# Kernel optimization log

Hardware: AMD Instinct MI355X
Metric: run time of the kernel (lower is better)

Reference implementation:

```python
import jax, jax.numpy as jnp
import numpy as np

# Dims (match init_kwargs)
B, N, D_MODEL = 64, 64, 512
D_STATE = 512
D_ATT = D_MODEL
H, W, C, K = 128, 128, 16, 5
T = 32  # num_steps
HALF = K // 2


def _lin(key, out_d, in_d):
    kw, kb = jax.random.split(key)
    w = jax.random.normal(kw, (out_d, in_d), jnp.float32) * 0.02
    b = jax.random.normal(kb, (out_d,), jnp.float32) * 0.02
    return w, b


def setup_inputs() -> dict:
    key = jax.random.key(0)
    ks = jax.random.split(key, 12)
    token_reps = jax.random.normal(ks[0], (B, N, D_MODEL), jnp.float32)
    global_rep = jax.random.normal(ks[1], (B, D_MODEL), jnp.float32)
    attention_mask = jnp.ones((B, N), jnp.int32)
    w_init, b_init = _lin(ks[2], D_STATE, D_MODEL)
    wq, bq = _lin(ks[3], D_ATT, D_STATE)
    wk, bk = _lin(ks[4], D_ATT, D_MODEL)
    wv, bv = _lin(ks[5], D_ATT, D_MODEL)
    gru_in = D_ATT + D_MODEL
    w_ih, b_ih = _lin(ks[6], 3 * D_STATE, gru_in)
    w_hh, b_hh = _lin(ks[7], 3 * D_STATE, D_STATE)
    w_write, b_write = _lin(ks[8], C * K * K, D_STATE + D_ATT)
    w_loc, b_loc = _lin(ks[9], 3, D_STATE + D_ATT + D_MODEL)
    return dict(token_reps=token_reps, global_rep=global_rep, attention_mask=attention_mask,
                w_init=w_init, b_init=b_init, wq=wq, bq=bq, wk=wk, bk=bk, wv=wv, bv=bv,
                w_ih=w_ih, b_ih=b_ih, w_hh=w_hh, b_hh=b_hh,
                w_write=w_write, b_write=b_write, w_loc=w_loc, b_loc=b_loc)


def _forward(token_reps, global_rep, attention_mask,
             w_init, b_init, wq, bq, wk, bk, wv, bv,
             w_ih, b_ih, w_hh, b_hh, w_write, b_write, w_loc, b_loc):
    Bv = token_reps.shape[0]
    # Precompute keys/values (constant over steps)
    k_tok = token_reps @ wk.T + bk  # [B,N,d_att]
    v_tok = token_reps @ wv.T + bv  # [B,N,d_att]
    invalid = attention_mask == 0

    s0 = jnp.tanh(global_rep @ w_init.T + b_init)  # [B,d_state]
    # Padded canvas (NHWC): full KxK patches always fit; crop at the end
    # reproduces the torch clipped-window write exactly.
    canvas0 = jnp.zeros((Bv, H + 2 * HALF, W + 2 * HALF, C), jnp.float32)
    b_idx = jnp.arange(Bv)
    koff = jnp.arange(K)

    def step(carry, _):
        s, canvas_p = carry
        q = s @ wq.T + bq  # [B,d_att]
        scores = jnp.einsum('bd,bnd->bn', q, k_tok)
        scores = jnp.where(invalid, -1e9, scores)
        alpha = jax.nn.softmax(scores, axis=-1)
        r = jnp.einsum('bn,bnd->bd', alpha, v_tok)  # [B,d_att]
        # GRUCell (torch gate order r,z,n)
        x = jnp.concatenate([r, global_rep], axis=-1)
        gi = x @ w_ih.T + b_ih
        gh = s @ w_hh.T + b_hh
        ir, iz, inn = jnp.split(gi, 3, axis=-1)
        hr, hz, hn = jnp.split(gh, 3, axis=-1)
        rg = jax.nn.sigmoid(ir + hr)
        zg = jax.nn.sigmoid(iz + hz)
        ng = jnp.tanh(inn + rg * hn)
        s_new = (1.0 - zg) * ng + zg * s
        # Write patch
        patch = (jnp.concatenate([s_new, r], axis=-1) @ w_write.T + b_write)
        patch = patch.reshape(Bv, C, K, K).transpose(0, 2, 3, 1)  # [B,K,K,C]
        loc = jnp.concatenate([s_new, r, global_rep], axis=-1) @ w_loc.T + b_loc
        cx = jnp.tanh(loc[:, 0])
        cy = jnp.tanh(loc[:, 1])
        j = jnp.clip(jnp.round(0.5 * (cx + 1.0) * (W - 1)), 0, W - 1).astype(jnp.int32)
        i = jnp.clip(jnp.round(0.5 * (cy + 1.0) * (H - 1)), 0, H - 1).astype(jnp.int32)
        # padded coords: top-left of window in padded canvas is (i, j)
        rows = i[:, None] + koff  # [B,K]
        cols = j[:, None] + koff  # [B,K]
        canvas_p = canvas_p.at[b_idx[:, None, None], rows[:, :, None], cols[:, None, :]].add(patch)
        return (s_new, canvas_p), None

    (_, canvas_p), _ = jax.lax.scan(step, (s0, canvas0), None, length=T)
    canvas = canvas_p[:, HALF:HALF + H, HALF:HALF + W, :].transpose(0, 3, 1, 2)  # [B,C,H,W]
    return canvas


def reference(token_reps, global_rep, attention_mask,
              w_init, b_init, wq, bq, wk, bk, wv, bv,
              w_ih, b_ih, w_hh, b_hh, w_write, b_write, w_loc, b_loc):
    return _forward(token_reps, global_rep, attention_mask,
                    w_init, b_init, wq, bq, wk, bk, wv, bv,
                    w_ih, b_ih, w_hh, b_hh, w_write, b_write, w_loc, b_loc)
```

## Files before the change

kernel.cpp:

```cpp
#include <hip/hip_runtime.h>

#define BB 64
#define DD 512
#define TT 32

__device__ __forceinline__ float dot4(const float4 a, const float4 b) {
  return a.x * b.x + a.y * b.y + a.z * b.z + a.w * b.w;
}

__device__ __forceinline__ void cst(float* p, float v) {
  __hip_atomic_store(p, v, __ATOMIC_RELAXED, __HIP_MEMORY_SCOPE_AGENT);
}

__global__ void vecs_k(const float* __restrict__ wq, const float* __restrict__ bk,
                       const float* __restrict__ wk, const float* __restrict__ bq,
                       float* __restrict__ kqb, float* __restrict__ wkbq,
                       float* __restrict__ bqbk, unsigned* __restrict__ bar) {
  const int tid = threadIdx.x, bz = blockIdx.x;
  if (bz < 2) {
    const int d = bz * 256 + tid;
    float s = 0.f;
    for (int e = 0; e < DD; ++e) s += wq[e * DD + d] * bk[e];
    kqb[d] = s;
  } else {
    const int k = (bz - 2) * 256 + tid;
    float s = 0.f;
    for (int e = 0; e < DD; ++e) s += bq[e] * wk[e * DD + k];
    wkbq[k] = s;
    if (bz == 2 && tid == 0) {
      float t2 = 0.f;
      for (int e = 0; e < DD; ++e) t2 += bq[e] * bk[e];
      *bqbk = t2;
    }
    if (bz == 3) {
      if (tid < 16)
        __hip_atomic_store(bar + tid * 64, 0u, __ATOMIC_RELAXED, __HIP_MEMORY_SCOPE_AGENT);
      __hip_atomic_store(bar + 1024 + tid * 32, 0u, __ATOMIC_RELAXED, __HIP_MEMORY_SCOPE_AGENT);
    }
  }
}

__global__ __launch_bounds__(256) void gemm128_k(
    const float* __restrict__ A, int lda, int a_trans,
    const float* __restrict__ B, int ldb, int boff, int b_trans,
    const float* __restrict__ bias, float* __restrict__ C, long c_stride_z, int ldc,
    int kfrom, int klen, int act) {
  __shared__ __align__(16) float As[16][132];
  __shared__ __align__(16) float Bs[16][68];
  const int tid = threadIdx.x;
  const int tx = tid & 15, ty = tid >> 4;
  const int m0 = blockIdx.x * 128, n0 = blockIdx.y * 64;
  const int kbase = kfrom + blockIdx.z * klen;
  float* Ce = C + (long)blockIdx.z * c_stride_z;
  float acc[8][4];
#pragma unroll
  for (int i = 0; i < 8; ++i)
#pragma unroll
    for (int j = 0; j < 4; ++j) acc[i][j] = 0.f;

  for (int k0 = kbase; k0 < kbase + klen; k0 += 16) {
    if (!a_trans) {
      const int row = tid >> 1, half = tid & 1;
      const float* ap = A + (long)(m0 + row) * lda + k0 + half * 8;
      const float4 a0 = *(const float4*)ap;
      const float4 a1 = *(const float4*)(ap + 4);
      const int kb = half * 8;
      As[kb + 0][row] = a0.x; As[kb + 1][row] = a0.y; As[kb + 2][row] = a0.z; As[kb + 3][row] = a0.w;
      As[kb + 4][row] = a1.x; As[kb + 5][row] = a1.y; As[kb + 6][row] = a1.z; As[kb + 7][row] = a1.w;
    } else {
      const int kk = tid >> 4, mseg = tid & 15;
      const float* ap = A + (long)(k0 + kk) * lda + m0 + mseg * 8;
      *(float4*)&As[kk][mseg * 8] = *(const float4*)ap;
      *(float4*)&As[kk][mseg * 8 + 4] = *(const float4*)(ap + 4);
    }
    if (!b_trans) {
      const int n = tid >> 2, q = tid & 3;
      const float4 b0 = *(const float4*)(B + (long)(n0 + n) * ldb + boff + k0 + q * 4);
      Bs[q * 4 + 0][n] = b0.x; Bs[q * 4 + 1][n] = b0.y; Bs[q * 4 + 2][n] = b0.z; Bs[q * 4 + 3][n] = b0.w;
    } else {
      const int kk = tid >> 4, nq = tid & 15;
      *(float4*)&Bs[kk][nq * 4] = *(const float4*)(B + (long)(k0 + kk) * ldb + boff + n0 + nq * 4);
    }
    __syncthreads();
#pragma unroll
    for (int kk = 0; kk < 16; ++kk) {
      const float4 a0 = *(const float4*)&As[kk][ty * 8];
      const float4 a1 = *(const float4*)&As[kk][ty * 8 + 4];
      const float4 b0 = *(const float4*)&Bs[kk][tx * 4];
      const float am[8] = {a0.x, a0.y, a0.z, a0.w, a1.x, a1.y, a1.z, a1.w};
#pragma unroll
      for (int i = 0; i < 8; ++i) {
        acc[i][0] += am[i] * b0.x; acc[i][1] += am[i] * b0.y;
        acc[i][2] += am[i] * b0.z; acc[i][3] += am[i] * b0.w;
      }
    }
    __syncthreads();
  }
  float4 bv = make_float4(0.f, 0.f, 0.f, 0.f);
  if (bias) bv = *(const float4*)(bias + n0 + tx * 4);
#pragma unroll
  for (int i = 0; i < 8; ++i) {
    const int m = m0 + ty * 8 + i;
    float4 v = make_float4(acc[i][0] + bv.x, acc[i][1] + bv.y, acc[i][2] + bv.z, acc[i][3] + bv.w);
    if (act == 1) { v.x = tanhf(v.x); v.y = tanhf(v.y); v.z = tanhf(v.z); v.w = tanhf(v.w); }
    *(float4*)&Ce[(long)m * ldc + n0 + tx * 4] = v;
  }
}

__global__ __launch_bounds__(256) void gemm128_dual_k(
    const float* __restrict__ A,
    const float* __restrict__ B0, const float* __restrict__ bias0, float* __restrict__ C0,
    const float* __restrict__ B1, const float* __restrict__ bias1, float* __restrict__ C1) {
  __shared__ __align__(16) float As[16][132];
  __shared__ __align__(16) float Bs[16][68];
  const int tid = threadIdx.x;
  const int tx = tid & 15, ty = tid >> 4;
  const int m0 = blockIdx.x * 128, n0 = blockIdx.y * 64;
  const float* B = blockIdx.z ? B1 : B0;
  const float* bias = blockIdx.z ? bias1 : bias0;
  float* C = blockIdx.z ? C1 : C0;
  float acc[8][4];
#pragma unroll
  for (int i = 0; i < 8; ++i)
#pragma unroll
    for (int j = 0; j < 4; ++j) acc[i][j] = 0.f;

  for (int k0 = 0; k0 < 512; k0 += 16) {
    {
      const int row = tid >> 1, half = tid & 1;
      const float* ap = A + (long)(m0 + row) * 512 + k0 + half * 8;
      const float4 a0 = *(const float4*)ap;
      const float4 a1 = *(const float4*)(ap + 4);
      const int kb = half * 8;
      As[kb + 0][row] = a0.x; As[kb + 1][row] = a0.y; As[kb + 2][row] = a0.z; As[kb + 3][row] = a0.w;
      As[kb + 4][row] = a1.x; As[kb + 5][row] = a1.y; As[kb + 6][row] = a1.z; As[kb + 7][row] = a1.w;
    }
    {
      const int n = tid >> 2, q = tid & 3;
      const float4 b0 = *(const float4*)(B + (long)(n0 + n) * 512 + k0 + q * 4);
      Bs[q * 4 + 0][n] = b0.x; Bs[q * 4 + 1][n] = b0.y; Bs[q * 4 + 2][n] = b0.z; Bs[q * 4 + 3][n] = b0.w;
    }
    __syncthreads();
#pragma unroll
    for (int kk = 0; kk < 16; ++kk) {
      const float4 a0 = *(const float4*)&As[kk][ty * 8];
      const float4 a1 = *(const float4*)&As[kk][ty * 8 + 4];
      const float4 b0 = *(const float4*)&Bs[kk][tx * 4];
      const float am[8] = {a0.x, a0.y, a0.z, a0.w, a1.x, a1.y, a1.z, a1.w};
#pragma unroll
      for (int i = 0; i < 8; ++i) {
        acc[i][0] += am[i] * b0.x; acc[i][1] += am[i] * b0.y;
        acc[i][2] += am[i] * b0.z; acc[i][3] += am[i] * b0.w;
      }
    }
    __syncthreads();
  }
  const float4 bvv = *(const float4*)(bias + n0 + tx * 4);
#pragma unroll
  for (int i = 0; i < 8; ++i) {
    const int m = m0 + ty * 8 + i;
    float4 v = make_float4(acc[i][0] + bvv.x, acc[i][1] + bvv.y, acc[i][2] + bvv.z, acc[i][3] + bvv.w);
    *(float4*)&C[(long)m * 512 + n0 + tx * 4] = v;
  }
}

__global__ void combine4_k(const float* __restrict__ p, float* __restrict__ out) {
  const int i = blockIdx.x * blockDim.x + threadIdx.x;
  const float4 a = ((const float4*)p)[i];
  const float4 b = ((const float4*)p)[i + 65536];
  const float4 c = ((const float4*)p)[i + 131072];
  const float4 d = ((const float4*)p)[i + 196608];
  ((float4*)out)[i] = make_float4(a.x + b.x + c.x + d.x, a.y + b.y + c.y + d.y,
                                  a.z + b.z + c.z + d.z, a.w + b.w + c.w + d.w);
}

__device__ __forceinline__ void grid_barrier(unsigned* __restrict__ bar, unsigned gen) {
  __syncthreads();
  const int blk = blockIdx.x, tid = threadIdx.x;
  unsigned* gctr = bar;
  unsigned* rel = bar + 1024;
  if (blk == 0) {
    if (tid == 0)
      __hip_atomic_fetch_add(gctr, 1u, __ATOMIC_RELAXED, __HIP_MEMORY_SCOPE_AGENT);
    if (tid < 16) {
      while (__hip_atomic_load(gctr + tid * 64, __ATOMIC_RELAXED, __HIP_MEMORY_SCOPE_AGENT) < gen * 16u)
        __builtin_amdgcn_s_sleep(1);
    }
    __syncthreads();
    __hip_atomic_store(rel + tid * 32, gen, __ATOMIC_RELAXED, __HIP_MEMORY_SCOPE_AGENT);
  } else {
    if (tid == 0) {
      __hip_atomic_fetch_add(gctr + (blk >> 4) * 64, 1u, __ATOMIC_RELAXED, __HIP_MEMORY_SCOPE_AGENT);
      while (__hip_atomic_load(rel + blk * 32, __ATOMIC_RELAXED, __HIP_MEMORY_SCOPE_AGENT) < gen)
        __builtin_amdgcn_s_sleep(1);
    }
  }
  __syncthreads();
}

__global__ __launch_bounds__(256, 1) void loop_k(
    const float* __restrict__ ktil, float* __restrict__ cbn,
    const float* __restrict__ vt, float* __restrict__ locg,
    float* __restrict__ sbuf, float* __restrict__ rbuf,
    const float* __restrict__ w_write, const float* __restrict__ b_write,
    const float* __restrict__ w_loc, const int* __restrict__ amask,
    float* __restrict__ patchbuf, float* __restrict__ locbuf,
    float* __restrict__ gig, const float* __restrict__ w_ih,
    const float* __restrict__ w_hh, const float* __restrict__ b_hh,
    unsigned* __restrict__ bar,
    const float* __restrict__ tok, const float* __restrict__ grep,
    const float* __restrict__ wkbq, const float* __restrict__ bqbk,
    const float* __restrict__ w_init, const float* __restrict__ b_init,
    const float* __restrict__ b_ih, const float* __restrict__ b_loc) {
  __shared__ __align__(16) float smem[10048];
  __shared__ __align__(16) float wpl[12288];
  float* sm_act = smem;
  float* sm_val = smem + 9216;
  float* sm_sc  = smem + 9408;
  float* sm_s   = smem;
  float* sm_r   = smem + 4608;
  float* sm_g   = smem + 9216;

  const int blk = blockIdx.x, tid = threadIdx.x, lane = tid & 63;
  const bool is_attn = (blk < 64);
  const bool is_patch = (blk >= 64) && (blk < 224);
  unsigned nsync = 0;

  if (blk < 16) {
    for (int i = tid; i < 512; i += 256) smem[i] = wkbq[i];
    __syncthreads();
    const int m = blk * 256 + tid;
    const float* tr = tok + (long)m * 512;
    float acc = bqbk[0];
    for (int e = 0; e < 512; e += 8) {
      acc += dot4(*(const float4*)(tr + e), *(const float4*)(smem + e));
      acc += dot4(*(const float4*)(tr + e + 4), *(const float4*)(smem + e + 4));
    }
    cst(cbn + m, acc);
    __syncthreads();
  } else if (blk < 40) {
    const int o = (blk - 16) * 64 + (tid & 63);
    const int b0 = (tid >> 6) * 16;
    float acc[16];
#pragma unroll
    for (int i = 0; i < 16; ++i) acc[i] = 0.f;
    const float* wr = w_ih + (long)o * 1024 + 512;
    for (int e = 0; e < 512; e += 4) {
      const float4 w4 = *(const float4*)(wr + e);
#pragma unroll
      for (int i = 0; i < 16; ++i)
        acc[i] += dot4(*(const float4*)(grep + (long)(b0 + i) * 512 + e), w4);
    }
    const float bi = b_ih[o];
#pragma unroll
    for (int i = 0; i < 16; ++i)
      cst(gig + (long)(b0 + i) * 1536 + o, acc[i] + bi);
  } else if (blk < 48) {
    const int d = (blk - 40) * 64 + (tid & 63);
    const int b0 = (tid >> 6) * 16;
    float acc[16];
#pragma unroll
    for (int i = 0; i < 16; ++i) acc[i] = 0.f;
    const float* wr = w_init + (long)d * 512;
    for (int e = 0; e < 512; e += 4) {
      const float4 w4 = *(const float4*)(wr + e);
#pragma unroll
      for (int i = 0; i < 16; ++i)
        acc[i] += dot4(*(const float4*)(grep + (long)(b0 + i) * 512 + e), w4);
    }
    const float bi = b_init[d];
#pragma unroll
    for (int i = 0; i < 16; ++i)
      cst(sbuf + (long)(b0 + i) * 512 + d, tanhf(acc[i] + bi));
  } else if (blk == 48) {
    if (tid < 128) {
      const int b = tid >> 1, j = tid & 1;
      const float* wr = w_loc + (long)j * 1536 + 1024;
      const float* gr = grep + (long)b * 512;
      float acc = b_loc[j];
      for (int e = 0; e < 512; e += 4)
        acc += dot4(*(const float4*)(gr + e), *(const float4*)(wr + e));
      cst(locg + b * 2 + j, acc);
    }
  }

  int p_rg = 0, p_bg = 0;
  if (is_patch) {
    const int g = blk - 64;
    p_bg = g & 3; p_rg = g >> 2;
    for (int idx = tid; idx < 3072; idx += 256) {
      const int rho = idx >> 8, f4 = idx & 255;
      const int col = f4 << 2;
      const int cc2 = col >> 5, jj = (col >> 2) & 7;
      const int dcol = (cc2 << 5) | ((jj ^ (cc2 & 7)) << 2);
      const float* src = (rho < 10) ? (w_write + (long)(p_rg * 10 + rho) * 1024 + col)
                                    : (w_loc + (long)(rho - 10) * 1536 + col);
      *(float4*)(wpl + rho * 1024 + dcol) = *(const float4*)src;
    }
  }

  float4 wg[3][8];
  const int g_dg = blk & 63, g_bg = blk >> 6;
  {
    const int c = tid & 15, sl = tid >> 4;
#pragma unroll
    for (int i = 0; i < 3; ++i) {
      const int rho = sl * 3 + i;
      const float* wsrc;
      if (rho < 24) {
        const int g2 = rho >> 3, di = rho & 7;
        wsrc = w_ih + (long)(g2 * 512 + g_dg * 8 + di) * 1024 + c * 32;
      } else {
        const int rh = rho - 24, g2 = rh >> 3, di = rh & 7;
        wsrc = w_hh + (long)(g2 * 512 + g_dg * 8 + di) * 512 + c * 32;
      }
#pragma unroll
      for (int j = 0; j < 8; ++j) wg[i][j] = *(const float4*)(wsrc + 4 * j);
    }
  }

  grid_barrier(bar, ++nsync);

  for (int t = 0; t <= TT; ++t) {
    const float* s_cur = sbuf + (long)t * (BB * DD);
    float* r_cur = rbuf + (long)t * (BB * DD);
    const float* r_prev = r_cur - BB * DD;

    if (is_attn) {
      if (t < TT) {
        const int b = blk, wrp = tid >> 6;
        const float* sb = s_cur + (long)b * DD;
        const float4 sva = *(const float4*)(sb + lane * 8);
        const float4 svb = *(const float4*)(sb + lane * 8 + 4);
        for (int h8 = 0; h8 < 2; ++h8) {
          const float* kbase = ktil + ((long)(b * 64 + wrp * 16 + h8 * 8)) * DD + lane * 8;
          float4 ka[8], kb2[8];
#pragma unroll
          for (int i = 0; i < 8; ++i) {
            ka[i] = *(const float4*)(kbase + (long)i * DD);
            kb2[i] = *(const float4*)(kbase + (long)i * DD + 4);
          }
#pragma unroll
          for (int i = 0; i < 8; ++i) {
            float p = dot4(ka[i], sva) + dot4(kb2[i], svb);
#pragma unroll
            for (int off = 32; off; off >>= 1) p += __shfl_xor(p, off);
            if (lane == 0) {
              const int n = wrp * 16 + h8 * 8 + i;
              float sc = p + cbn[b * 64 + n];
              if (amask[b * 64 + n] == 0) sc = -1e9f;
              sm_sc[n] = sc;
            }
          }
        }
        __syncthreads();
        if (tid < 64) {
          const float v = sm_sc[tid];
          float m = v;
#pragma unroll
          for (int off = 32; off; off >>= 1) m = fmaxf(m, __shfl_xor(m, off));
          const float e = expf(v - m);
          float l2 = e;
#pragma unroll
          for (int off = 32; off; off >>= 1) l2 += __shfl_xor(l2, off);
          sm_sc[tid] = e / l2;
        }
        __syncthreads();
        float rx = 0.f, ry = 0.f;
        const float* vb = vt + (long)b * 64 * DD + (tid << 1);
        for (int n0 = 0; n0 < 64; n0 += 8) {
          float2 vv[8];
#pragma unroll
          for (int i = 0; i < 8; ++i)
            vv[i] = *(const float2*)(vb + (long)(n0 + i) * DD);
#pragma unroll
          for (int i = 0; i < 8; ++i) {
            const float a = sm_sc[n0 + i];
            rx = fmaf(a, vv[i].x, rx);
            ry = fmaf(a, vv[i].y, ry);
          }
        }
        cst(r_cur + (long)b * DD + (tid << 1), rx);
        cst(r_cur + (long)b * DD + (tid << 1) + 1, ry);
      }
    } else if (is_patch) {
      if (t >= 1) {
        const int c = tid & 31, sl = tid >> 5;
        const int tr = sl & 3, bgsub = sl >> 2;
        for (int h = 0; h < 2; ++h) {
          __syncthreads();
          {
            const int b_i8 = tid >> 5, l = tid & 31;
            const int b = p_bg * 16 + h * 8 + b_i8;
            const float* sp = s_cur + (long)b * DD + l * 16;
            const float* rp = r_prev + (long)b * DD + l * 16;
            float* dsd = sm_act + b_i8 * 1152 + (l >> 1) * 36 + (l & 1) * 16;
            float* drd = sm_act + b_i8 * 1152 + (16 + (l >> 1)) * 36 + (l & 1) * 16;
#pragma unroll
            for (int jj = 0; jj < 4; ++jj) {
              *(float4*)(dsd + 4 * jj) = *(const float4*)(sp + 4 * jj);
              *(float4*)(drd + 4 * jj) = *(const float4*)(rp + 4 * jj);
            }
          }
          __syncthreads();
          float4 wreg[3][8];
#pragma unroll
          for (int i = 0; i < 3; ++i) {
            const float* wrow = wpl + (tr * 3 + i) * 1024 + (c << 5);
#pragma unroll
            for (int j = 0; j < 8; ++j)
              wreg[i][j] = *(const float4*)(wrow + ((j ^ (c & 7)) << 2));
          }
          for (int bi = 0; bi < 4; ++bi) {
            const int bl = bgsub * 4 + bi;
            const int babs = p_bg * 16 + h * 8 + bl;
            const float* ap = sm_act + bl * 1152 + c * 36;
            float a0 = 0.f, a1 = 0.f, a2 = 0.f;
#pragma unroll
            for (int j = 0; j < 8; ++j) {
              const float4 av = *(const float4*)(ap + 4 * j);
              a0 += dot4(wreg[0][j], av);
              a1 += dot4(wreg[1][j], av);
              a2 += dot4(wreg[2][j], av);
            }
#pragma unroll
            for (int m = 1; m < 32; m <<= 1) {
              a0 += __shfl_xor(a0, m);
              a1 += __shfl_xor(a1, m);
              a2 += __shfl_xor(a2, m);
            }
            if (c == 0) {
              const int bslot = h * 8 + bl;
              const float av3[3] = {a0, a1, a2};
#pragma unroll
              for (int i = 0; i < 3; ++i) {
                const int rho = tr * 3 + i;
                float v = av3[i];
                if (rho >= 10) v += locg[babs * 2 + (rho - 10)];
                sm_val[rho * 16 + bslot] = v;
              }
            }
          }
        }
        __syncthreads();
        const int u = t - 1;
        if (tid < 160) {
          const int ri = tid >> 4, bl2 = tid & 15;
          const int row = p_rg * 10 + ri;
          const int b = p_bg * 16 + bl2;
          patchbuf[((long)u * 64 + b) * 400 + row] = sm_val[ri * 16 + bl2] + b_write[row];
        }
        if (p_rg == 0 && tid < 16) {
          const int b = p_bg * 16 + tid;
          const float lx = sm_val[160 + tid];
          const float ly = sm_val[176 + tid];
          const int jx = min(127, max(0, (int)rintf(0.5f * (tanhf(lx) + 1.f) * 127.f)));
          const int iy = min(127, max(0, (int)rintf(0.5f * (tanhf(ly) + 1.f) * 127.f)));
          locbuf[((long)u * 64 + b) * 2] = (float)jx;
          locbuf[((long)u * 64 + b) * 2 + 1] = (float)iy;
        }
      }
    }

    if (t == TT) break;

    grid_barrier(bar, ++nsync);

    {
      float* s_nxt = sbuf + (long)(t + 1) * (BB * DD);
      const int c = tid & 15, sl = tid >> 4;
      for (int h = 0; h < 2; ++h) {
        __syncthreads();
        {
          const int b_i8 = tid >> 5, l = tid & 31;
          const int b = g_bg * 16 + h * 8 + b_i8;
          const float* sp = s_cur + (long)b * DD + l * 16;
          const float* rp = r_cur + (long)b * DD + l * 16;
          float* dsd = sm_s + b_i8 * 576 + (l >> 1) * 36 + (l & 1) * 16;
          float* drd = sm_r + b_i8 * 576 + (l >> 1) * 36 + (l & 1) * 16;
#pragma unroll
          for (int jj = 0; jj < 4; ++jj) {
            *(float4*)(dsd + 4 * jj) = *(const float4*)(sp + 4 * jj);
            *(float4*)(drd + 4 * jj) = *(const float4*)(rp + 4 * jj);
          }
        }
        __syncthreads();
        const float* base = (sl < 8) ? sm_r : sm_s;
        for (int bl = 0; bl < 8; ++bl) {
          const float* ap = base + bl * 576 + c * 36;
          float a0 = 0.f, a1 = 0.f, a2 = 0.f;
#pragma unroll
          for (int j = 0; j < 8; ++j) {
            const float4 av = *(const float4*)(ap + 4 * j);
            a0 += dot4(wg[0][j], av);
            a1 += dot4(wg[1][j], av);
            a2 += dot4(wg[2][j], av);
          }
#pragma unroll
          for (int m = 1; m < 16; m <<= 1) {
            a0 += __shfl_xor(a0, m);
            a1 += __shfl_xor(a1, m);
            a2 += __shfl_xor(a2, m);
          }
          if (c == 0) {
            const int bslot = h * 8 + bl;
            sm_g[bslot * 52 + sl * 3 + 0] = a0;
            sm_g[bslot * 52 + sl * 3 + 1] = a1;
            sm_g[bslot * 52 + sl * 3 + 2] = a2;
          }
        }
      }
      __syncthreads();
      if (tid < 128) {
        const int b_i = tid >> 3, di = tid & 7;
        const int b = g_bg * 16 + b_i, d = g_dg * 8 + di;
        const float ir = sm_g[b_i * 52 + di]        + gig[b * 1536 + d];
        const float iz = sm_g[b_i * 52 + 8 + di]    + gig[b * 1536 + 512 + d];
        const float in = sm_g[b_i * 52 + 16 + di]   + gig[b * 1536 + 1024 + d];
        const float hr = sm_g[b_i * 52 + 24 + di]   + b_hh[d];
        const float hz = sm_g[b_i * 52 + 32 + di]   + b_hh[512 + d];
        const float hn = sm_g[b_i * 52 + 40 + di]   + b_hh[1024 + d];
        const float rg2 = 1.f / (1.f + expf(-(ir + hr)));
        const float zg = 1.f / (1.f + expf(-(iz + hz)));
        const float ng = tanhf(in + rg2 * hn);
        const float sprev = s_cur[(long)b * DD + d];
        cst(s_nxt + (long)b * DD + d, (1.f - zg) * ng + zg * sprev);
      }
    }

    grid_barrier(bar, ++nsync);
  }
}

__global__ __launch_bounds__(256) void canvas_k(const float* __restrict__ pb,
                                                const float* __restrict__ lb,
                                                float* __restrict__ canvas) {
  __shared__ float ch[16384];
  const int blk = blockIdx.x, tid = threadIdx.x;
  const int b = blk >> 4, c = blk & 15;
  for (int i = tid; i < 4096; i += 256)
    ((float4*)ch)[i] = make_float4(0.f, 0.f, 0.f, 0.f);
  __syncthreads();
  for (int u = 0; u < TT; ++u) {
    const int jx = (int)lb[((long)u * 64 + b) * 2];
    const int iy = (int)lb[((long)u * 64 + b) * 2 + 1];
    if (tid < 25) {
      const float v = pb[((long)u * 64 + b) * 400 + c * 25 + tid];
      const int ki = tid / 5, kj = tid % 5;
      const int y = iy + ki - 2, x = jx + kj - 2;
      if (y >= 0 && y < 128 && x >= 0 && x < 128) ch[y * 128 + x] += v;
    }
    __syncthreads();
  }
  float* dst = canvas + ((long)b * 16 + c) * 16384;
  for (int i = tid; i < 4096; i += 256)
    ((float4*)dst)[i] = ((float4*)ch)[i];
}

extern "C" void kernel_launch(void* const* d_in, const int* in_sizes, int n_in,
                              void* d_out, int out_size, void* d_ws, size_t ws_size,
                              hipStream_t stream) {
  const float* tok     = (const float*)d_in[0];
  const float* grep    = (const float*)d_in[1];
  const int*   amask   = (const int*)d_in[2];
  const float* w_init  = (const float*)d_in[3];
  const float* b_init  = (const float*)d_in[4];
  const float* wq      = (const float*)d_in[5];
  const float* bq      = (const float*)d_in[6];
  const float* wk      = (const float*)d_in[7];
  const float* bk      = (const float*)d_in[8];
  const float* wv      = (const float*)d_in[9];
  const float* bv      = (const float*)d_in[10];
  const float* w_ih    = (const float*)d_in[11];
  const float* b_ih    = (const float*)d_in[12];
  const float* w_hh    = (const float*)d_in[13];
  const float* b_hh    = (const float*)d_in[14];
  const float* w_write = (const float*)d_in[15];
  const float* b_write = (const float*)d_in[16];
  const float* w_loc   = (const float*)d_in[17];
  const float* b_loc   = (const float*)d_in[18];
  float* canvas = (float*)d_out;

  float* ws = (float*)d_ws;
  float* ktil = ws;
  float* vtw  = ktil + 2097152;
  float* Aqk  = vtw + 2097152;
  float* gig  = Aqk + 262144;
  float* cbn  = gig + 98304;
  float* sbuf = cbn + 4096;
  float* rbuf = sbuf + 1081344;
  float* locg = rbuf + 1048576;
  float* kqb  = locg + 128;
  float* wkbq = kqb + 512;
  float* bqbk = wkbq + 512;
  unsigned* bar = (unsigned*)(bqbk + 64);
  float* patchbuf = (float*)(bar + 16384);
  float* locbuf = patchbuf + 819200;

  vecs_k<<<4, 256, 0, stream>>>(wq, bk, wk, bq, kqb, wkbq, bqbk, bar);
  gemm128_k<<<dim3(4, 8, 4), 256, 0, stream>>>(wq, 512, 1, wk, 512, 0, 1,
                                               nullptr, vtw, 262144L, 512, 0, 128, 0);
  combine4_k<<<256, 256, 0, stream>>>(vtw, Aqk);
  gemm128_dual_k<<<dim3(32, 8, 2), 256, 0, stream>>>(tok, Aqk, kqb, ktil, wv, bv, vtw);

  loop_k<<<256, 256, 0, stream>>>(ktil, cbn, vtw, locg, sbuf, rbuf, w_write, b_write,
                                  w_loc, amask, patchbuf, locbuf, gig, w_ih, w_hh, b_hh, bar,
                                  tok, grep, wkbq, bqbk, w_init, b_init, b_ih, b_loc);
  canvas_k<<<1024, 256, 0, stream>>>(patchbuf, locbuf, canvas);
}
```

Baseline: 1.107 ms.

## Merge setup kernels and move per-batch precompute out of persistent loop kernel

The split-K Wq·Wk GEMM, the bias vector products, the cbn/gig/s0/locg precomputations and the barrier reset are merged into one setup kernel. The four-way partial-sum combine is folded into the B-tile load of the dual GEMM, and aqkp partials are stored in the rbuf region. This removes two launches, the combine kernel and one grid-wide barrier inside the persistent loop kernel. The trade-offs are some redundant reduction work across the setup blocks, and the extra reads of four partial buffers repeated in every dual-GEMM block, which re-reads the sums many times.

Result: faster. 1.082 ms (-2.3%).

```diff
diff --git a/kernel.cpp b/kernel.cpp
--- a/kernel.cpp
+++ b/kernel.cpp
@@ -12,113 +12,152 @@
   __hip_atomic_store(p, v, __ATOMIC_RELAXED, __HIP_MEMORY_SCOPE_AGENT);
 }
 
-__global__ void vecs_k(const float* __restrict__ wq, const float* __restrict__ bk,
-                       const float* __restrict__ wk, const float* __restrict__ bq,
-                       float* __restrict__ kqb, float* __restrict__ wkbq,
-                       float* __restrict__ bqbk, unsigned* __restrict__ bar) {
-  const int tid = threadIdx.x, bz = blockIdx.x;
-  if (bz < 2) {
-    const int d = bz * 256 + tid;
+__global__ __launch_bounds__(256) void setup_k(
+    const float* __restrict__ wq, const float* __restrict__ bq,
+    const float* __restrict__ wk, const float* __restrict__ bk,
+    const float* __restrict__ tok, const float* __restrict__ grep,
+    const float* __restrict__ w_ih, const float* __restrict__ b_ih,
+    const float* __restrict__ w_init, const float* __restrict__ b_init,
+    const float* __restrict__ w_loc, const float* __restrict__ b_loc,
+    float* __restrict__ kqb, float* __restrict__ cbn, float* __restrict__ gig,
+    float* __restrict__ sbuf, float* __restrict__ locg,
+    float* __restrict__ aqkp, unsigned* __restrict__ bar) {
+  __shared__ __align__(16) float As[16][132];
+  __shared__ __align__(16) float Bs[16][68];
+  const int blk = blockIdx.x, tid = threadIdx.x;
+
+  if (blk < 128) {
+    const int tx = tid & 15, ty = tid >> 4;
+    const int m0 = (blk & 3) * 128, n0 = ((blk >> 2) & 7) * 64, zz = blk >> 5;
+    float acc[8][4];
+#pragma unroll
+    for (int i = 0; i < 8; ++i)
+#pragma unroll
+      for (int j = 0; j < 4; ++j) acc[i][j] = 0.f;
+    for (int k0 = zz * 128; k0 < zz * 128 + 128; k0 += 16) {
+      {
+        const int kk = tid >> 4, mseg = tid & 15;
+        const float* ap = wq + (long)(k0 + kk) * 512 + m0 + mseg * 8;
+        *(float4*)&As[kk][mseg * 8] = *(const float4*)ap;
+        *(float4*)&As[kk][mseg * 8 + 4] = *(const float4*)(ap + 4);
+      }
+      {
+        const int kk = tid >> 4, nq = tid & 15;
+        *(float4*)&Bs[kk][nq * 4] = *(const float4*)(wk + (long)(k0 + kk) * 512 + n0 + nq * 4);
+      }
+      __syncthreads();
+#pragma unroll
+      for (int kk = 0; kk < 16; ++kk) {
+        const float4 a0 = *(const float4*)&As[kk][ty * 8];
+        const float4 a1 = *(const float4*)&As[kk][ty * 8 + 4];
+        const float4 b0 = *(const float4*)&Bs[kk][tx * 4];
+        const float am[8] = {a0.x, a0.y, a0.z, a0.w, a1.x, a1.y, a1.z, a1.w};
+#pragma unroll
+        for (int i = 0; i < 8; ++i) {
+          acc[i][0] += am[i] * b0.x; acc[i][1] += am[i] * b0.y;
+          acc[i][2] += am[i] * b0.z; acc[i][3] += am[i] * b0.w;
+        }
+      }
+      __syncthreads();
+    }
+    float* Ce = aqkp + (long)zz * 262144;
+#pragma unroll
+    for (int i = 0; i < 8; ++i) {
+      const int m = m0 + ty * 8 + i;
+      *(float4*)&Ce[(long)m * 512 + n0 + tx * 4] =
+          make_float4(acc[i][0], acc[i][1], acc[i][2], acc[i][3]);
+    }
+  } else if (blk < 130) {
+    const int d = (blk - 128) * 256 + tid;
     float s = 0.f;
     for (int e = 0; e < DD; ++e) s += wq[e * DD + d] * bk[e];
     kqb[d] = s;
+  } else if (blk < 146) {
+    float* wkb = &As[0][0];
+    float* red = &Bs[0][0];
+    for (int k = tid; k < 512; k += 256) {
+      float s = 0.f;
+      for (int e = 0; e < DD; ++e) s += bq[e] * wk[e * DD + k];
+      wkb[k] = s;
+    }
+    red[tid] = bq[tid] * bk[tid] + bq[tid + 256] * bk[tid + 256];
+    __syncthreads();
+    for (int s2 = 128; s2; s2 >>= 1) {
+      if (tid < s2) red[tid] += red[tid + s2];
+      __syncthreads();
+    }
+    const float bqbk = red[0];
+    const int m = (blk - 130) * 256 + tid;
+    const float* tr = tok + (long)m * 512;
+    float acc = bqbk;
+    for (int e = 0; e < 512; e += 8) {
+      acc += dot4(*(const float4*)(tr + e), *(const float4*)(wkb + e));
+      acc += dot4(*(const float4*)(tr + e + 4), *(const float4*)(wkb + e + 4));
+    }
+    cbn[m] = acc;
+  } else if (blk < 170) {
+    const int o = (blk - 146) * 64 + (tid & 63);
+    const int b0 = (tid >> 6) * 16;
+    float acc[16];
+#pragma unroll
+    for (int i = 0; i < 16; ++i) acc[i] = 0.f;
+    const float* wr = w_ih + (long)o * 1024 + 512;
+    for (int e = 0; e < 512; e += 4) {
+      const float4 w4 = *(const float4*)(wr + e);
+#pragma unroll
+      for (int i = 0; i < 16; ++i)
+        acc[i] += dot4(*(const float4*)(grep + (long)(b0 + i) * 512 + e), w4);
+    }
+    const float bi = b_ih[o];
+#pragma unroll
+    for (int i = 0; i < 16; ++i)
+      gig[(long)(b0 + i) * 1536 + o] = acc[i] + bi;
+  } else if (blk < 178) {
+    const int d = (blk - 170) * 64 + (tid & 63);
+    const int b0 = (tid >> 6) * 16;
+    float acc[16];
+#pragma unroll
+    for (int i = 0; i < 16; ++i) acc[i] = 0.f;
+    const float* wr = w_init + (long)d * 512;
+    for (int e = 0; e < 512; e += 4) {
+      const float4 w4 = *(const float4*)(wr + e);
+#pragma unroll
+      for (int i = 0; i < 16; ++i)
+        acc[i] += dot4(*(const float4*)(grep + (long)(b0 + i) * 512 + e), w4);
+    }
+    const float bi = b_init[d];
+#pragma unroll
+    for (int i = 0; i < 16; ++i)
+      sbuf[(long)(b0 + i) * 512 + d] = tanhf(acc[i] + bi);
+  } else if (blk == 178) {
+    if (tid < 128) {
+      const int b = tid >> 1, j = tid & 1;
+      const float* wr = w_loc + (long)j * 1536 + 1024;
+      const float* gr = grep + (long)b * 512;
+      float acc = b_loc[j];
+      for (int e = 0; e < 512; e += 4)
+        acc += dot4(*(const float4*)(gr + e), *(const float4*)(wr + e));
+      locg[b * 2 + j] = acc;
+    }
   } else {
-    const int k = (bz - 2) * 256 + tid;
-    float s = 0.f;
-    for (int e = 0; e < DD; ++e) s += bq[e] * wk[e * DD + k];
-    wkbq[k] = s;
-    if (bz == 2 && tid == 0) {
-      float t2 = 0.f;
-      for (int e = 0; e < DD; ++e) t2 += bq[e] * bk[e];
-      *bqbk = t2;
-    }
-    if (bz == 3) {
-      if (tid < 16)
-        __hip_atomic_store(bar + tid * 64, 0u, __ATOMIC_RELAXED, __HIP_MEMORY_SCOPE_AGENT);
-      __hip_atomic_store(bar + 1024 + tid * 32, 0u, __ATOMIC_RELAXED, __HIP_MEMORY_SCOPE_AGENT);
-    }
-  }
-}
-
-__global__ __launch_bounds__(256) void gemm128_k(
-    const float* __restrict__ A, int lda, int a_trans,
-    const float* __restrict__ B, int ldb, int boff, int b_trans,
-    const float* __restrict__ bias, float* __restrict__ C, long c_stride_z, int ldc,
-    int kfrom, int klen, int act) {
-  __shared__ __align__(16) float As[16][132];
-  __shared__ __align__(16) float Bs[16][68];
-  const int tid = threadIdx.x;
-  const int tx = tid & 15, ty = tid >> 4;
-  const int m0 = blockIdx.x * 128, n0 = blockIdx.y * 64;
-  const int kbase = kfrom + blockIdx.z * klen;
-  float* Ce = C + (long)blockIdx.z * c_stride_z;
-  float acc[8][4];
-#pragma unroll
-  for (int i = 0; i < 8; ++i)
-#pragma unroll
-    for (int j = 0; j < 4; ++j) acc[i][j] = 0.f;
-
-  for (int k0 = kbase; k0 < kbase + klen; k0 += 16) {
-    if (!a_trans) {
-      const int row = tid >> 1, half = tid & 1;
-      const float* ap = A + (long)(m0 + row) * lda + k0 + half * 8;
-      const float4 a0 = *(const float4*)ap;
-      const float4 a1 = *(const float4*)(ap + 4);
-      const int kb = half * 8;
-      As[kb + 0][row] = a0.x; As[kb + 1][row] = a0.y; As[kb + 2][row] = a0.z; As[kb + 3][row] = a0.w;
-      As[kb + 4][row] = a1.x; As[kb + 5][row] = a1.y; As[kb + 6][row] = a1.z; As[kb + 7][row] = a1.w;
-    } else {
-      const int kk = tid >> 4, mseg = tid & 15;
-      const float* ap = A + (long)(k0 + kk) * lda + m0 + mseg * 8;
-      *(float4*)&As[kk][mseg * 8] = *(const float4*)ap;
-      *(float4*)&As[kk][mseg * 8 + 4] = *(const float4*)(ap + 4);
-    }
-    if (!b_trans) {
-      const int n = tid >> 2, q = tid & 3;
-      const float4 b0 = *(const float4*)(B + (long)(n0 + n) * ldb + boff + k0 + q * 4);
-      Bs[q * 4 + 0][n] = b0.x; Bs[q * 4 + 1][n] = b0.y; Bs[q * 4 + 2][n] = b0.z; Bs[q * 4 + 3][n] = b0.w;
-    } else {
-      const int kk = tid >> 4, nq = tid & 15;
-      *(float4*)&Bs[kk][nq * 4] = *(const float4*)(B + (long)(k0 + kk) * ldb + boff + n0 + nq * 4);
-    }
-    __syncthreads();
-#pragma unroll
-    for (int kk = 0; kk < 16; ++kk) {
-      const float4 a0 = *(const float4*)&As[kk][ty * 8];
-      const float4 a1 = *(const float4*)&As[kk][ty * 8 + 4];
-      const float4 b0 = *(const float4*)&Bs[kk][tx * 4];
-      const float am[8] = {a0.x, a0.y, a0.z, a0.w, a1.x, a1.y, a1.z, a1.w};
-#pragma unroll
-      for (int i = 0; i < 8; ++i) {
-        acc[i][0] += am[i] * b0.x; acc[i][1] += am[i] * b0.y;
-        acc[i][2] += am[i] * b0.z; acc[i][3] += am[i] * b0.w;
-      }
-    }
-    __syncthreads();
-  }
-  float4 bv = make_float4(0.f, 0.f, 0.f, 0.f);
-  if (bias) bv = *(const float4*)(bias + n0 + tx * 4);
-#pragma unroll
-  for (int i = 0; i < 8; ++i) {
-    const int m = m0 + ty * 8 + i;
-    float4 v = make_float4(acc[i][0] + bv.x, acc[i][1] + bv.y, acc[i][2] + bv.z, acc[i][3] + bv.w);
-    if (act == 1) { v.x = tanhf(v.x); v.y = tanhf(v.y); v.z = tanhf(v.z); v.w = tanhf(v.w); }
-    *(float4*)&Ce[(long)m * ldc + n0 + tx * 4] = v;
-  }
-}
-
-__global__ __launch_bounds__(256) void gemm128_dual_k(
-    const float* __restrict__ A,
-    const float* __restrict__ B0, const float* __restrict__ bias0, float* __restrict__ C0,
+    if (tid < 16)
+      __hip_atomic_store(bar + tid * 64, 0u, __ATOMIC_RELAXED, __HIP_MEMORY_SCOPE_AGENT);
+    __hip_atomic_store(bar + 1024 + tid * 32, 0u, __ATOMIC_RELAXED, __HIP_MEMORY_SCOPE_AGENT);
+  }
+}
+
+__global__ __launch_bounds__(256) void dual2_k(
+    const float* __restrict__ A, const float* __restrict__ aqkp,
+    const float* __restrict__ bias0, float* __restrict__ C0,
     const float* __restrict__ B1, const float* __restrict__ bias1, float* __restrict__ C1) {
   __shared__ __align__(16) float As[16][132];
   __shared__ __align__(16) float Bs[16][68];
   const int tid = threadIdx.x;
   const int tx = tid & 15, ty = tid >> 4;
   const int m0 = blockIdx.x * 128, n0 = blockIdx.y * 64;
-  const float* B = blockIdx.z ? B1 : B0;
-  const float* bias = blockIdx.z ? bias1 : bias0;
-  float* C = blockIdx.z ? C1 : C0;
+  const int z = blockIdx.z;
+  const float* bias = z ? bias1 : bias0;
+  float* C = z ? C1 : C0;
   float acc[8][4];
 #pragma unroll
   for (int i = 0; i < 8; ++i)
@@ -137,7 +176,18 @@
     }
     {
       const int n = tid >> 2, q = tid & 3;
-      const float4 b0 = *(const float4*)(B + (long)(n0 + n) * 512 + k0 + q * 4);
+      float4 b0;
+      if (z == 0) {
+        const float* pb = aqkp + (long)(n0 + n) * 512 + k0 + q * 4;
+        const float4 p0 = *(const float4*)pb;
+        const float4 p1 = *(const float4*)(pb + 262144);
+        const float4 p2 = *(const float4*)(pb + 524288);
+        const float4 p3 = *(const float4*)(pb + 786432);
+        b0 = make_float4(p0.x + p1.x + p2.x + p3.x, p0.y + p1.y + p2.y + p3.y,
+                         p0.z + p1.z + p2.z + p3.z, p0.w + p1.w + p2.w + p3.w);
+      } else {
+        b0 = *(const float4*)(B1 + (long)(n0 + n) * 512 + k0 + q * 4);
+      }
       Bs[q * 4 + 0][n] = b0.x; Bs[q * 4 + 1][n] = b0.y; Bs[q * 4 + 2][n] = b0.z; Bs[q * 4 + 3][n] = b0.w;
     }
     __syncthreads();
@@ -162,16 +212,6 @@
     float4 v = make_float4(acc[i][0] + bvv.x, acc[i][1] + bvv.y, acc[i][2] + bvv.z, acc[i][3] + bvv.w);
     *(float4*)&C[(long)m * 512 + n0 + tx * 4] = v;
   }
-}
-
-__global__ void combine4_k(const float* __restrict__ p, float* __restrict__ out) {
-  const int i = blockIdx.x * blockDim.x + threadIdx.x;
-  const float4 a = ((const float4*)p)[i];
-  const float4 b = ((const float4*)p)[i + 65536];
-  const float4 c = ((const float4*)p)[i + 131072];
-  const float4 d = ((const float4*)p)[i + 196608];
-  ((float4*)out)[i] = make_float4(a.x + b.x + c.x + d.x, a.y + b.y + c.y + d.y,
-                                  a.z + b.z + c.z + d.z, a.w + b.w + c.w + d.w);
 }
 
 __device__ __forceinline__ void grid_barrier(unsigned* __restrict__ bar, unsigned gen) {
@@ -199,19 +239,15 @@
 }
 
 __global__ __launch_bounds__(256, 1) void loop_k(
-    const float* __restrict__ ktil, float* __restrict__ cbn,
-    const float* __restrict__ vt, float* __restrict__ locg,
+    const float* __restrict__ ktil, const float* __restrict__ cbn,
+    const float* __restrict__ vt, const float* __restrict__ locg,
     float* __restrict__ sbuf, float* __restrict__ rbuf,
     const float* __restrict__ w_write, const float* __restrict__ b_write,
     const float* __restrict__ w_loc, const int* __restrict__ amask,
     float* __restrict__ patchbuf, float* __restrict__ locbuf,
-    float* __restrict__ gig, const float* __restrict__ w_ih,
+    const float* __restrict__ gig, const float* __restrict__ w_ih,
     const float* __restrict__ w_hh, const float* __restrict__ b_hh,
-    unsigned* __restrict__ bar,
-    const float* __restrict__ tok, const float* __restrict__ grep,
-    const float* __restrict__ wkbq, const float* __restrict__ bqbk,
-    const float* __restrict__ w_init, const float* __restrict__ b_init,
-    const float* __restrict__ b_ih, const float* __restrict__ b_loc) {
+    unsigned* __restrict__ bar) {
   __shared__ __align__(16) float smem[10048];
   __shared__ __align__(16) float wpl[12288];
   float* sm_act = smem;
@@ -225,64 +261,6 @@
   const bool is_attn = (blk < 64);
   const bool is_patch = (blk >= 64) && (blk < 224);
   unsigned nsync = 0;
-
-  if (blk < 16) {
-    for (int i = tid; i < 512; i += 256) smem[i] = wkbq[i];
-    __syncthreads();
-    const int m = blk * 256 + tid;
-    const float* tr = tok + (long)m * 512;
-    float acc = bqbk[0];
-    for (int e = 0; e < 512; e += 8) {
-      acc += dot4(*(const float4*)(tr + e), *(const float4*)(smem + e));
-      acc += dot4(*(const float4*)(tr + e + 4), *(const float4*)(smem + e + 4));
-    }
-    cst(cbn + m, acc);
-    __syncthreads();
-  } else if (blk < 40) {
-    const int o = (blk - 16) * 64 + (tid & 63);
-    const int b0 = (tid >> 6) * 16;
-    float acc[16];
-#pragma unroll
-    for (int i = 0; i < 16; ++i) acc[i] = 0.f;
-    const float* wr = w_ih + (long)o * 1024 + 512;
-    for (int e = 0; e < 512; e += 4) {
-      const float4 w4 = *(const float4*)(wr + e);
-#pragma unroll
-      for (int i = 0; i < 16; ++i)
-        acc[i] += dot4(*(const float4*)(grep + (long)(b0 + i) * 512 + e), w4);
-    }
-    const float bi = b_ih[o];
-#pragma unroll
-    for (int i = 0; i < 16; ++i)
-      cst(gig + (long)(b0 + i) * 1536 + o, acc[i] + bi);
-  } else if (blk < 48) {
-    const int d = (blk - 40) * 64 + (tid & 63);
-    const int b0 = (tid >> 6) * 16;
-    float acc[16];
-#pragma unroll
-    for (int i = 0; i < 16; ++i) acc[i] = 0.f;
-    const float* wr = w_init + (long)d * 512;
-    for (int e = 0; e < 512; e += 4) {
-      const float4 w4 = *(const float4*)(wr + e);
-#pragma unroll
-      for (int i = 0; i < 16; ++i)
-        acc[i] += dot4(*(const float4*)(grep + (long)(b0 + i) * 512 + e), w4);
-    }
-    const float bi = b_init[d];
-#pragma unroll
-    for (int i = 0; i < 16; ++i)
-      cst(sbuf + (long)(b0 + i) * 512 + d, tanhf(acc[i] + bi));
-  } else if (blk == 48) {
-    if (tid < 128) {
-      const int b = tid >> 1, j = tid & 1;
-      const float* wr = w_loc + (long)j * 1536 + 1024;
-      const float* gr = grep + (long)b * 512;
-      float acc = b_loc[j];
-      for (int e = 0; e < 512; e += 4)
-        acc += dot4(*(const float4*)(gr + e), *(const float4*)(wr + e));
-      cst(locg + b * 2 + j, acc);
-    }
-  }
 
   int p_rg = 0, p_bg = 0;
   if (is_patch) {
@@ -318,8 +296,7 @@
       for (int j = 0; j < 8; ++j) wg[i][j] = *(const float4*)(wsrc + 4 * j);
     }
   }
-
-  grid_barrier(bar, ++nsync);
+  __syncthreads();
 
   for (int t = 0; t <= TT; ++t) {
     const float* s_cur = sbuf + (long)t * (BB * DD);
@@ -596,15 +573,13 @@
   unsigned* bar = (unsigned*)(bqbk + 64);
   float* patchbuf = (float*)(bar + 16384);
   float* locbuf = patchbuf + 819200;
-
-  vecs_k<<<4, 256, 0, stream>>>(wq, bk, wk, bq, kqb, wkbq, bqbk, bar);
-  gemm128_k<<<dim3(4, 8, 4), 256, 0, stream>>>(wq, 512, 1, wk, 512, 0, 1,
-                                               nullptr, vtw, 262144L, 512, 0, 128, 0);
-  combine4_k<<<256, 256, 0, stream>>>(vtw, Aqk);
-  gemm128_dual_k<<<dim3(32, 8, 2), 256, 0, stream>>>(tok, Aqk, kqb, ktil, wv, bv, vtw);
-
+  float* aqkp = rbuf;
+
+  setup_k<<<180, 256, 0, stream>>>(wq, bq, wk, bk, tok, grep, w_ih, b_ih,
+                                   w_init, b_init, w_loc, b_loc,
+                                   kqb, cbn, gig, sbuf, locg, aqkp, bar);
+  dual2_k<<<dim3(32, 8, 2), 256, 0, stream>>>(tok, aqkp, kqb, ktil, wv, bv, vtw);
   loop_k<<<256, 256, 0, stream>>>(ktil, cbn, vtw, locg, sbuf, rbuf, w_write, b_write,
-                                  w_loc, amask, patchbuf, locbuf, gig, w_ih, w_hh, b_hh, bar,
-                                  tok, grep, wkbq, bqbk, w_init, b_init, b_ih, b_loc);
+                                  w_loc, amask, patchbuf, locbuf, gig, w_ih, w_hh, b_hh, bar);
   canvas_k<<<1024, 256, 0, stream>>>(patchbuf, locbuf, canvas);
 }
```
